# Kernel optimization log

Measured on AMD Instinct MI355X. Metric: run time of the kernel, lower is better.

The kernel has to match this reference:

```python
import jax, jax.numpy as jnp
import numpy as np

BETA = 0.25
NUM_CODEBOOK = 1024
DIM = 256


def setup_inputs() -> dict:
    key = jax.random.key(0)
    k1, k2 = jax.random.split(key)
    z = jax.random.normal(k1, (32, DIM, 32, 32), dtype=jnp.float32)
    # nn.init.uniform_(weight, -1/num_codebook, 1/num_codebook)
    bound = 1.0 / NUM_CODEBOOK
    codebook = jax.random.uniform(k2, (NUM_CODEBOOK, DIM), dtype=jnp.float32,
                                  minval=-bound, maxval=bound)
    return {"z": z, "codebook": codebook}


def reference(z, codebook):
    B, C, H, W = z.shape
    # NCHW -> NHWC -> [B*H*W, C]
    z_flat = jnp.transpose(z, (0, 2, 3, 1)).reshape(-1, C)
    # squared euclidean distances to each code: [B*H*W, K]
    dist = (jnp.sum(z_flat * z_flat, axis=1, keepdims=True)
            + jnp.sum(codebook * codebook, axis=1)
            - 2.0 * jnp.matmul(z_flat, codebook.T))
    idx = jnp.argmin(dist, axis=-1)                      # [B*H*W]
    z_q = codebook[idx].reshape(B, H, W, C)              # gather
    z_q = jnp.transpose(z_q, (0, 3, 1, 2))               # back to NCHW
    commit_loss = (jnp.mean((jax.lax.stop_gradient(z_q) - z) ** 2)
                   + BETA * jnp.mean((z_q - jax.lax.stop_gradient(z)) ** 2))
    # straight-through estimator
    z_q_st = z + jax.lax.stop_gradient(z_q - z)
    return z_q_st, commit_loss
```

## Files before the change

kernel.cpp:

```cpp
#include <hip/hip_runtime.h>
#include <hip/hip_bf16.h>
#include <hip/hip_fp8.h>
#include <stdint.h>


#define WS_CN    0
#define WS_CB    4096
#define WS_PENC  266240
#define WS_PART2 790528
#define WS_PART  791040

typedef float f32x4 __attribute__((ext_vector_type(4)));
typedef long  i64;
typedef long  l64x2 __attribute__((ext_vector_type(2)));

template <bool HI>
static __device__ __forceinline__ unsigned pk2(float a, float b, unsigned old) {
#if __has_builtin(__builtin_amdgcn_cvt_pk_fp8_f32)
    return (unsigned)__builtin_amdgcn_cvt_pk_fp8_f32(a, b, (int)old, HI);
#else
    __hip_fp8_e4m3 qa(a), qb(b);
    unsigned w = (unsigned)qa.__x | ((unsigned)qb.__x << 8);
    return HI ? ((old & 0x0000FFFFu) | (w << 16)) : ((old & 0xFFFF0000u) | w);
#endif
}

__global__ __launch_bounds__(512) void k0_prep(const float* __restrict__ cb,
                                               float* __restrict__ cn256,
                                               unsigned char* __restrict__ cbf8) {
    const int w = threadIdx.x >> 6;
    const int l = threadIdx.x & 63;
    const int code = blockIdx.x * 8 + w;
    const float4 v = ((const float4*)cb)[code * 64 + l];
    float nrm = v.x * v.x + v.y * v.y + v.z * v.z + v.w * v.w;
    #pragma unroll
    for (int off = 1; off < 64; off <<= 1) nrm += __shfl_xor(nrm, off);
    if (l == 0) cn256[code] = 256.f * nrm;
    unsigned u = pk2<false>(-512.f * v.x, -512.f * v.y, 0u);
    u = pk2<true>(-512.f * v.z, -512.f * v.w, u);
    const int q = code >> 8, chunk = (code >> 4) & 15, r16 = code & 15;
    const int ks = l >> 3, kp = l >> 4, g4 = (l >> 1) & 3;
    const int lane = g4 * 16 + r16;
    const int byteoff = q * 65536 + ((chunk * 4 + kp) * 64 + lane) * 16
                      + (ks & 1) * 8 + (l & 1) * 4;
    *(unsigned*)(cbf8 + byteoff) = u;
}

__global__ __launch_bounds__(512) void k1_main(const float* __restrict__ z,
                                               const unsigned char* __restrict__ cbf8,
                                               const float* __restrict__ cn256,
                                               float* __restrict__ penc,
                                               float* __restrict__ part2) {
    __shared__ __align__(16) unsigned char lds[65536];
    const int t = threadIdx.x, w = t >> 6, l = t & 63;
    const int col = l & 15, g4 = l >> 4, gc4 = g4 * 4;
    const int b = blockIdx.x, q = b >> 7, grp = b & 127;
    const int img = grp >> 2, hw0 = (grp & 3) << 8;

    {
        const unsigned char* src = cbf8 + q * 65536;
        #pragma unroll
        for (int i = 0; i < 8; ++i) {
            const int off = i * 8192 + w * 1024;
            __builtin_amdgcn_global_load_lds(
                (const __attribute__((address_space(1))) unsigned*)(src + off + l * 16),
                (__attribute__((address_space(3))) unsigned*)(lds + off), 16, 0, 0);
        }
    }

    const float* zp = z + img * 262144 + hw0 + w * 32;
    float z2 = 0.f;
    i64 zf[2][8];
    #pragma unroll
    for (int pf = 0; pf < 2; ++pf) {
        const int p = pf * 16 + col;
        #pragma unroll
        for (int ks = 0; ks < 8; ++ks) {
            const float* s0 = zp + (ks * 32 + g4 * 8) * 1024 + p;
            float v0 = s0[0], v1 = s0[1024], v2 = s0[2048], v3 = s0[3072];
            float v4 = s0[4096], v5 = s0[5120], v6 = s0[6144], v7 = s0[7168];
            z2 += v0*v0 + v1*v1 + v2*v2 + v3*v3 + v4*v4 + v5*v5 + v6*v6 + v7*v7;
            unsigned lo = pk2<false>(v0, v1, 0u); lo = pk2<true>(v2, v3, lo);
            unsigned hi = pk2<false>(v4, v5, 0u); hi = pk2<true>(v6, v7, hi);
            zf[pf][ks] = (i64)(((unsigned long)hi << 32) | (unsigned long)lo);
        }
    }
    __syncthreads();

    float menc0 = __builtin_bit_cast(float, 0x7F7FFC00u);
    float menc1 = __builtin_bit_cast(float, 0x7F7FFC00u);

    i64 A0[8], A1[8];
#define LDA(DST, c) do {                                                         \
    _Pragma("unroll") for (int kp = 0; kp < 4; ++kp) {                           \
        l64x2 u = *(const l64x2*)(lds + (((c) * 4 + kp) * 64 + l) * 16);         \
        DST[2 * kp] = u.x; DST[2 * kp + 1] = u.y;                                \
    }                                                                            \
} while (0)
#define BODY(CUR, NXT, c) do {                                                   \
    if ((c) + 1 < 16) LDA(NXT, (c) + 1);                                         \
    f32x4 a0 = {0.f,0.f,0.f,0.f}, a1 = {0.f,0.f,0.f,0.f};                        \
    _Pragma("unroll") for (int ks = 0; ks < 8; ++ks) {                           \
        a0 = __builtin_amdgcn_mfma_f32_16x16x32_fp8_fp8(CUR[ks], zf[0][ks], a0, 0, 0, 0); \
        a1 = __builtin_amdgcn_mfma_f32_16x16x32_fp8_fp8(CUR[ks], zf[1][ks], a1, 0, 0, 0); \
    }                                                                            \
    {                                                                            \
        const f32x4 cn = *(const f32x4*)(cn256 + q * 256 + (c) * 16 + gc4);      \
        _Pragma("unroll") for (int r = 0; r < 4; ++r) {                          \
            const unsigned code0 = (unsigned)(q * 256 + (c) * 16 + gc4 + r);     \
            float s; unsigned e;                                                 \
            s = a0[r] + cn[r];                                                   \
            e = (__builtin_bit_cast(unsigned, s) & 0xFFFFFC00u) | code0;         \
            menc0 = fminf(menc0, __builtin_bit_cast(float, e));                  \
            s = a1[r] + cn[r];                                                   \
            e = (__builtin_bit_cast(unsigned, s) & 0xFFFFFC00u) | code0;         \
            menc1 = fminf(menc1, __builtin_bit_cast(float, e));                  \
        }                                                                        \
    }                                                                            \
} while (0)

    LDA(A0, 0);
    #pragma unroll 1
    for (int c2 = 0; c2 < 16; c2 += 2) {
        BODY(A0, A1, c2);
        BODY(A1, A0, c2 + 1);
    }
#undef BODY
#undef LDA

    menc0 = fminf(menc0, __shfl_xor(menc0, 16));
    menc0 = fminf(menc0, __shfl_xor(menc0, 32));
    menc1 = fminf(menc1, __shfl_xor(menc1, 16));
    menc1 = fminf(menc1, __shfl_xor(menc1, 32));
    const int posbase = img * 1024 + hw0 + w * 32;
    if (l < 16) {
        penc[q * 32768 + posbase + l]      = menc0;
        penc[q * 32768 + posbase + 16 + l] = menc1;
    }

    #pragma unroll
    for (int off = 1; off < 64; off <<= 1) z2 += __shfl_xor(z2, off);
    __syncthreads();
    float* red = (float*)lds;
    if (l == 0) red[w] = z2;
    __syncthreads();
    if (t == 0 && q == 0) {
        float s = 0.f;
        #pragma unroll
        for (int i = 0; i < 8; ++i) s += red[i];
        part2[grp] = s;
    }
}

__global__ __launch_bounds__(256) void k2_out(const float* __restrict__ cbf,
                                              const float* __restrict__ penc,
                                              float* __restrict__ out,
                                              float* __restrict__ part) {
    __shared__ __align__(16) float zqbuf[32 * 260];
    __shared__ unsigned idxl[64];
    const int t = threadIdx.x, b = blockIdx.x;
    const int pos0 = b * 64, img = pos0 >> 10, hw0 = pos0 & 1023;

    if (t < 64) {
        const int pos = pos0 + t;
        const float e = fminf(fminf(penc[pos], penc[32768 + pos]),
                              fminf(penc[65536 + pos], penc[98304 + pos]));
        const unsigned eu = __builtin_bit_cast(unsigned, e);
        idxl[t] = eu & 0x3FFu;
        float myS = __builtin_bit_cast(float, eu & 0xFFFFFC00u);
        #pragma unroll
        for (int off = 1; off < 64; off <<= 1) myS += __shfl_xor(myS, off);
        if (t == 0) part[b] = myS * (1.f / 256.f);
    }

    const float4* cb4 = (const float4*)cbf;
    const int pq = t & 7;
    const int cg = t >> 3;
    for (int h = 0; h < 2; ++h) {
        __syncthreads();
        #pragma unroll
        for (int i = 0; i < 8; ++i) {
            const int flat = i * 256 + t;
            const int p = flat >> 6;
            const int qq = flat & 63;
            const unsigned code = idxl[h * 32 + p];
            *(float4*)&zqbuf[p * 260 + qq * 4] = cb4[code * 64 + qq];
        }
        __syncthreads();
        float* ob = out + img * 262144 + hw0 + h * 32 + pq * 4;
        #pragma unroll
        for (int i = 0; i < 8; ++i) {
            const int ch = i * 32 + cg;
            float4 v;
            v.x = zqbuf[(pq * 4 + 0) * 260 + ch];
            v.y = zqbuf[(pq * 4 + 1) * 260 + ch];
            v.z = zqbuf[(pq * 4 + 2) * 260 + ch];
            v.w = zqbuf[(pq * 4 + 3) * 260 + ch];
            *(float4*)(ob + ch * 1024) = v;
        }
    }
}

__global__ __launch_bounds__(256) void k3_red(const float* __restrict__ part2,
                                              const float* __restrict__ part,
                                              float* __restrict__ out) {
    __shared__ float red[256];
    const int t = threadIdx.x;
    float v = part[t] + part[t + 256];
    if (t < 128) v += part2[t];
    red[t] = v;
    __syncthreads();
    #pragma unroll
    for (int off = 128; off > 0; off >>= 1) {
        if (t < off) red[t] += red[t + off];
        __syncthreads();
    }
    if (t == 0) out[8388608] = 1.25f * red[0] / 8388608.f;
}

extern "C" void kernel_launch(void* const* d_in, const int* in_sizes, int n_in,
                              void* d_out, int out_size, void* d_ws, size_t ws_size,
                              hipStream_t stream) {
    const float* z  = (const float*)d_in[0];
    const float* cb = (const float*)d_in[1];
    float* out = (float*)d_out;
    unsigned char* ws = (unsigned char*)d_ws;
    float* cn256 = (float*)(ws + WS_CN);
    unsigned char* cbf8 = ws + WS_CB;
    float* penc  = (float*)(ws + WS_PENC);
    float* part2 = (float*)(ws + WS_PART2);
    float* part  = (float*)(ws + WS_PART);

    hipLaunchKernelGGL(k0_prep, dim3(128), dim3(512), 0, stream, cb, cn256, cbf8);
    hipLaunchKernelGGL(k1_main, dim3(512), dim3(512), 0, stream, z, cbf8, cn256, penc, part2);
    hipLaunchKernelGGL(k2_out,  dim3(512), dim3(256), 0, stream, cb, penc, out, part);
    hipLaunchKernelGGL(k3_red,  dim3(1), dim3(256), 0, stream, part2, part, out);
}
```

Baseline: 44.79 us.

## Split codebook into eighths, give each wave 64 positions in smaller blocks

The main distance kernel now splits the codebook into 8 slices of 128 codes instead of 4 of 256, and runs 1024 blocks of 256 threads with 32KB of LDS instead of 512 blocks of 512 threads with 64KB. Each wave now covers 64 positions with four accumulator sets, so every codebook fragment read from LDS feeds four MFMAs instead of two. The double-buffered A-fragment prefetch is dropped, and the partial-min workspace and the reduction in the output kernel grow to 8 slices. This trades more z loads and conversions (z is now re-read for 8 code slices) and higher register use for better reuse of each LDS read and more blocks per CU.

After: 61.41 us. 37.1% more time.

```diff
diff --git a/kernel.cpp b/kernel.cpp
--- a/kernel.cpp
+++ b/kernel.cpp
@@ -7,8 +7,8 @@
 #define WS_CN    0
 #define WS_CB    4096
 #define WS_PENC  266240
-#define WS_PART2 790528
-#define WS_PART  791040
+#define WS_PART2 1314816
+#define WS_PART  1315328
 
 typedef float f32x4 __attribute__((ext_vector_type(4)));
 typedef long  i64;
@@ -38,41 +38,42 @@
     if (l == 0) cn256[code] = 256.f * nrm;
     unsigned u = pk2<false>(-512.f * v.x, -512.f * v.y, 0u);
     u = pk2<true>(-512.f * v.z, -512.f * v.w, u);
-    const int q = code >> 8, chunk = (code >> 4) & 15, r16 = code & 15;
-    const int ks = l >> 3, kp = l >> 4, g4 = (l >> 1) & 3;
+    const int e = code >> 7, chunk = (code >> 4) & 7, r16 = code & 15;
+    const int kp = l >> 4, g4 = (l >> 1) & 3;
     const int lane = g4 * 16 + r16;
-    const int byteoff = q * 65536 + ((chunk * 4 + kp) * 64 + lane) * 16
-                      + (ks & 1) * 8 + (l & 1) * 4;
+    const int byteoff = e * 32768 + ((chunk * 4 + kp) * 64 + lane) * 16
+                      + ((l >> 3) & 1) * 8 + (l & 1) * 4;
     *(unsigned*)(cbf8 + byteoff) = u;
 }
 
-__global__ __launch_bounds__(512) void k1_main(const float* __restrict__ z,
+__global__ __launch_bounds__(256) void k1_main(const float* __restrict__ z,
                                                const unsigned char* __restrict__ cbf8,
                                                const float* __restrict__ cn256,
                                                float* __restrict__ penc,
                                                float* __restrict__ part2) {
-    __shared__ __align__(16) unsigned char lds[65536];
+    __shared__ __align__(16) unsigned char lds[32768];
+    __shared__ float redz[4];
     const int t = threadIdx.x, w = t >> 6, l = t & 63;
     const int col = l & 15, g4 = l >> 4, gc4 = g4 * 4;
-    const int b = blockIdx.x, q = b >> 7, grp = b & 127;
+    const int b = blockIdx.x, e = b >> 7, grp = b & 127;
     const int img = grp >> 2, hw0 = (grp & 3) << 8;
 
     {
-        const unsigned char* src = cbf8 + q * 65536;
+        const unsigned char* src = cbf8 + e * 32768;
         #pragma unroll
         for (int i = 0; i < 8; ++i) {
-            const int off = i * 8192 + w * 1024;
+            const int off = i * 4096 + w * 1024;
             __builtin_amdgcn_global_load_lds(
                 (const __attribute__((address_space(1))) unsigned*)(src + off + l * 16),
                 (__attribute__((address_space(3))) unsigned*)(lds + off), 16, 0, 0);
         }
     }
 
-    const float* zp = z + img * 262144 + hw0 + w * 32;
+    const float* zp = z + img * 262144 + hw0 + w * 64;
     float z2 = 0.f;
-    i64 zf[2][8];
-    #pragma unroll
-    for (int pf = 0; pf < 2; ++pf) {
+    i64 zf[4][8];
+    #pragma unroll
+    for (int pf = 0; pf < 4; ++pf) {
         const int p = pf * 16 + col;
         #pragma unroll
         for (int ks = 0; ks < 8; ++ks) {
@@ -89,67 +90,67 @@
 
     float menc0 = __builtin_bit_cast(float, 0x7F7FFC00u);
     float menc1 = __builtin_bit_cast(float, 0x7F7FFC00u);
-
-    i64 A0[8], A1[8];
-#define LDA(DST, c) do {                                                         \
-    _Pragma("unroll") for (int kp = 0; kp < 4; ++kp) {                           \
-        l64x2 u = *(const l64x2*)(lds + (((c) * 4 + kp) * 64 + l) * 16);         \
-        DST[2 * kp] = u.x; DST[2 * kp + 1] = u.y;                                \
-    }                                                                            \
-} while (0)
-#define BODY(CUR, NXT, c) do {                                                   \
-    if ((c) + 1 < 16) LDA(NXT, (c) + 1);                                         \
-    f32x4 a0 = {0.f,0.f,0.f,0.f}, a1 = {0.f,0.f,0.f,0.f};                        \
-    _Pragma("unroll") for (int ks = 0; ks < 8; ++ks) {                           \
-        a0 = __builtin_amdgcn_mfma_f32_16x16x32_fp8_fp8(CUR[ks], zf[0][ks], a0, 0, 0, 0); \
-        a1 = __builtin_amdgcn_mfma_f32_16x16x32_fp8_fp8(CUR[ks], zf[1][ks], a1, 0, 0, 0); \
-    }                                                                            \
-    {                                                                            \
-        const f32x4 cn = *(const f32x4*)(cn256 + q * 256 + (c) * 16 + gc4);      \
-        _Pragma("unroll") for (int r = 0; r < 4; ++r) {                          \
-            const unsigned code0 = (unsigned)(q * 256 + (c) * 16 + gc4 + r);     \
-            float s; unsigned e;                                                 \
-            s = a0[r] + cn[r];                                                   \
-            e = (__builtin_bit_cast(unsigned, s) & 0xFFFFFC00u) | code0;         \
-            menc0 = fminf(menc0, __builtin_bit_cast(float, e));                  \
-            s = a1[r] + cn[r];                                                   \
-            e = (__builtin_bit_cast(unsigned, s) & 0xFFFFFC00u) | code0;         \
-            menc1 = fminf(menc1, __builtin_bit_cast(float, e));                  \
-        }                                                                        \
-    }                                                                            \
-} while (0)
-
-    LDA(A0, 0);
+    float menc2 = __builtin_bit_cast(float, 0x7F7FFC00u);
+    float menc3 = __builtin_bit_cast(float, 0x7F7FFC00u);
+
     #pragma unroll 1
-    for (int c2 = 0; c2 < 16; c2 += 2) {
-        BODY(A0, A1, c2);
-        BODY(A1, A0, c2 + 1);
-    }
-#undef BODY
-#undef LDA
+    for (int c = 0; c < 8; ++c) {
+        i64 A[8];
+        #pragma unroll
+        for (int kp = 0; kp < 4; ++kp) {
+            l64x2 u = *(const l64x2*)(lds + ((c * 4 + kp) * 64 + l) * 16);
+            A[2 * kp] = u.x; A[2 * kp + 1] = u.y;
+        }
+        f32x4 a0 = {0.f,0.f,0.f,0.f}, a1 = {0.f,0.f,0.f,0.f};
+        f32x4 a2 = {0.f,0.f,0.f,0.f}, a3 = {0.f,0.f,0.f,0.f};
+        #pragma unroll
+        for (int ks = 0; ks < 8; ++ks) {
+            a0 = __builtin_amdgcn_mfma_f32_16x16x32_fp8_fp8(A[ks], zf[0][ks], a0, 0, 0, 0);
+            a1 = __builtin_amdgcn_mfma_f32_16x16x32_fp8_fp8(A[ks], zf[1][ks], a1, 0, 0, 0);
+            a2 = __builtin_amdgcn_mfma_f32_16x16x32_fp8_fp8(A[ks], zf[2][ks], a2, 0, 0, 0);
+            a3 = __builtin_amdgcn_mfma_f32_16x16x32_fp8_fp8(A[ks], zf[3][ks], a3, 0, 0, 0);
+        }
+        const f32x4 cn = *(const f32x4*)(cn256 + e * 128 + c * 16 + gc4);
+        #pragma unroll
+        for (int r = 0; r < 4; ++r) {
+            const unsigned code0 = (unsigned)(e * 128 + c * 16 + gc4 + r);
+            float s; unsigned u;
+            s = a0[r] + cn[r];
+            u = (__builtin_bit_cast(unsigned, s) & 0xFFFFFC00u) | code0;
+            menc0 = fminf(menc0, __builtin_bit_cast(float, u));
+            s = a1[r] + cn[r];
+            u = (__builtin_bit_cast(unsigned, s) & 0xFFFFFC00u) | code0;
+            menc1 = fminf(menc1, __builtin_bit_cast(float, u));
+            s = a2[r] + cn[r];
+            u = (__builtin_bit_cast(unsigned, s) & 0xFFFFFC00u) | code0;
+            menc2 = fminf(menc2, __builtin_bit_cast(float, u));
+            s = a3[r] + cn[r];
+            u = (__builtin_bit_cast(unsigned, s) & 0xFFFFFC00u) | code0;
+            menc3 = fminf(menc3, __builtin_bit_cast(float, u));
+        }
+    }
 
     menc0 = fminf(menc0, __shfl_xor(menc0, 16));
     menc0 = fminf(menc0, __shfl_xor(menc0, 32));
     menc1 = fminf(menc1, __shfl_xor(menc1, 16));
     menc1 = fminf(menc1, __shfl_xor(menc1, 32));
-    const int posbase = img * 1024 + hw0 + w * 32;
+    menc2 = fminf(menc2, __shfl_xor(menc2, 16));
+    menc2 = fminf(menc2, __shfl_xor(menc2, 32));
+    menc3 = fminf(menc3, __shfl_xor(menc3, 16));
+    menc3 = fminf(menc3, __shfl_xor(menc3, 32));
     if (l < 16) {
-        penc[q * 32768 + posbase + l]      = menc0;
-        penc[q * 32768 + posbase + 16 + l] = menc1;
+        const int pbase = e * 32768 + grp * 256 + w * 64;
+        penc[pbase + l]      = menc0;
+        penc[pbase + 16 + l] = menc1;
+        penc[pbase + 32 + l] = menc2;
+        penc[pbase + 48 + l] = menc3;
     }
 
     #pragma unroll
     for (int off = 1; off < 64; off <<= 1) z2 += __shfl_xor(z2, off);
+    if (l == 0) redz[w] = z2;
     __syncthreads();
-    float* red = (float*)lds;
-    if (l == 0) red[w] = z2;
-    __syncthreads();
-    if (t == 0 && q == 0) {
-        float s = 0.f;
-        #pragma unroll
-        for (int i = 0; i < 8; ++i) s += red[i];
-        part2[grp] = s;
-    }
+    if (t == 0 && e == 0) part2[grp] = redz[0] + redz[1] + redz[2] + redz[3];
 }
 
 __global__ __launch_bounds__(256) void k2_out(const float* __restrict__ cbf,
@@ -163,8 +164,11 @@
 
     if (t < 64) {
         const int pos = pos0 + t;
-        const float e = fminf(fminf(penc[pos], penc[32768 + pos]),
-                              fminf(penc[65536 + pos], penc[98304 + pos]));
+        const float e01 = fminf(penc[pos],          penc[32768 + pos]);
+        const float e23 = fminf(penc[65536 + pos],  penc[98304 + pos]);
+        const float e45 = fminf(penc[131072 + pos], penc[163840 + pos]);
+        const float e67 = fminf(penc[196608 + pos], penc[229376 + pos]);
+        const float e = fminf(fminf(e01, e23), fminf(e45, e67));
         const unsigned eu = __builtin_bit_cast(unsigned, e);
         idxl[t] = eu & 0x3FFu;
         float myS = __builtin_bit_cast(float, eu & 0xFFFFFC00u);
@@ -232,7 +236,7 @@
     float* part  = (float*)(ws + WS_PART);
 
     hipLaunchKernelGGL(k0_prep, dim3(128), dim3(512), 0, stream, cb, cn256, cbf8);
-    hipLaunchKernelGGL(k1_main, dim3(512), dim3(512), 0, stream, z, cbf8, cn256, penc, part2);
+    hipLaunchKernelGGL(k1_main, dim3(1024), dim3(256), 0, stream, z, cbf8, cn256, penc, part2);
     hipLaunchKernelGGL(k2_out,  dim3(512), dim3(256), 0, stream, cb, penc, out, part);
     hipLaunchKernelGGL(k3_red,  dim3(1), dim3(256), 0, stream, part2, part, out);
 }
```

## Split codebook into eight slices and use smaller blocks in main kernel

Applied to the files above, without the earlier changes.

Repartitions the distance/argmin kernel so each block handles 128 codes and 128 positions with 256 threads, giving 2048 blocks instead of 512 and halving LDS per block. The codebook FP8 layout, partial-argmin buffer (now eight slices), and the downstream merge and loss reduction are adjusted to match. This aims to raise occupancy and the number of waves across CUs. In exchange, each z tile is loaded and converted to FP8 by twice as many blocks, and the merge step reads more partial results.

Result: slower. 52.25 us (+16.7%).

```diff
diff --git a/kernel.cpp b/kernel.cpp
--- a/kernel.cpp
+++ b/kernel.cpp
@@ -7,8 +7,8 @@
 #define WS_CN    0
 #define WS_CB    4096
 #define WS_PENC  266240
-#define WS_PART2 790528
-#define WS_PART  791040
+#define WS_PART2 1314816
+#define WS_PART  1315840
 
 typedef float f32x4 __attribute__((ext_vector_type(4)));
 typedef long  i64;
@@ -38,30 +38,30 @@
     if (l == 0) cn256[code] = 256.f * nrm;
     unsigned u = pk2<false>(-512.f * v.x, -512.f * v.y, 0u);
     u = pk2<true>(-512.f * v.z, -512.f * v.w, u);
-    const int q = code >> 8, chunk = (code >> 4) & 15, r16 = code & 15;
-    const int ks = l >> 3, kp = l >> 4, g4 = (l >> 1) & 3;
+    const int e = code >> 7, chunk = (code >> 4) & 7, r16 = code & 15;
+    const int kp = l >> 4, g4 = (l >> 1) & 3;
     const int lane = g4 * 16 + r16;
-    const int byteoff = q * 65536 + ((chunk * 4 + kp) * 64 + lane) * 16
-                      + (ks & 1) * 8 + (l & 1) * 4;
+    const int byteoff = e * 32768 + ((chunk * 4 + kp) * 64 + lane) * 16
+                      + ((l >> 3) & 1) * 8 + (l & 1) * 4;
     *(unsigned*)(cbf8 + byteoff) = u;
 }
 
-__global__ __launch_bounds__(512) void k1_main(const float* __restrict__ z,
+__global__ __launch_bounds__(256) void k1_main(const float* __restrict__ z,
                                                const unsigned char* __restrict__ cbf8,
                                                const float* __restrict__ cn256,
                                                float* __restrict__ penc,
                                                float* __restrict__ part2) {
-    __shared__ __align__(16) unsigned char lds[65536];
+    __shared__ __align__(16) unsigned char lds[32768];
     const int t = threadIdx.x, w = t >> 6, l = t & 63;
     const int col = l & 15, g4 = l >> 4, gc4 = g4 * 4;
-    const int b = blockIdx.x, q = b >> 7, grp = b & 127;
-    const int img = grp >> 2, hw0 = (grp & 3) << 8;
+    const int b = blockIdx.x, e = b >> 8, grp = b & 255;
+    const int img = grp >> 3, hw0 = (grp & 7) << 7;
 
     {
-        const unsigned char* src = cbf8 + q * 65536;
+        const unsigned char* src = cbf8 + e * 32768;
         #pragma unroll
         for (int i = 0; i < 8; ++i) {
-            const int off = i * 8192 + w * 1024;
+            const int off = i * 4096 + w * 1024;
             __builtin_amdgcn_global_load_lds(
                 (const __attribute__((address_space(1))) unsigned*)(src + off + l * 16),
                 (__attribute__((address_space(3))) unsigned*)(lds + off), 16, 0, 0);
@@ -98,30 +98,30 @@
     }                                                                            \
 } while (0)
 #define BODY(CUR, NXT, c) do {                                                   \
-    if ((c) + 1 < 16) LDA(NXT, (c) + 1);                                         \
+    if ((c) + 1 < 8) LDA(NXT, (c) + 1);                                          \
     f32x4 a0 = {0.f,0.f,0.f,0.f}, a1 = {0.f,0.f,0.f,0.f};                        \
     _Pragma("unroll") for (int ks = 0; ks < 8; ++ks) {                           \
         a0 = __builtin_amdgcn_mfma_f32_16x16x32_fp8_fp8(CUR[ks], zf[0][ks], a0, 0, 0, 0); \
         a1 = __builtin_amdgcn_mfma_f32_16x16x32_fp8_fp8(CUR[ks], zf[1][ks], a1, 0, 0, 0); \
     }                                                                            \
     {                                                                            \
-        const f32x4 cn = *(const f32x4*)(cn256 + q * 256 + (c) * 16 + gc4);      \
+        const f32x4 cn = *(const f32x4*)(cn256 + e * 128 + (c) * 16 + gc4);      \
         _Pragma("unroll") for (int r = 0; r < 4; ++r) {                          \
-            const unsigned code0 = (unsigned)(q * 256 + (c) * 16 + gc4 + r);     \
-            float s; unsigned e;                                                 \
+            const unsigned code0 = (unsigned)(e * 128 + (c) * 16 + gc4 + r);     \
+            float s; unsigned u;                                                 \
             s = a0[r] + cn[r];                                                   \
-            e = (__builtin_bit_cast(unsigned, s) & 0xFFFFFC00u) | code0;         \
-            menc0 = fminf(menc0, __builtin_bit_cast(float, e));                  \
+            u = (__builtin_bit_cast(unsigned, s) & 0xFFFFFC00u) | code0;         \
+            menc0 = fminf(menc0, __builtin_bit_cast(float, u));                  \
             s = a1[r] + cn[r];                                                   \
-            e = (__builtin_bit_cast(unsigned, s) & 0xFFFFFC00u) | code0;         \
-            menc1 = fminf(menc1, __builtin_bit_cast(float, e));                  \
+            u = (__builtin_bit_cast(unsigned, s) & 0xFFFFFC00u) | code0;         \
+            menc1 = fminf(menc1, __builtin_bit_cast(float, u));                  \
         }                                                                        \
     }                                                                            \
 } while (0)
 
     LDA(A0, 0);
     #pragma unroll 1
-    for (int c2 = 0; c2 < 16; c2 += 2) {
+    for (int c2 = 0; c2 < 8; c2 += 2) {
         BODY(A0, A1, c2);
         BODY(A1, A0, c2 + 1);
     }
@@ -132,10 +132,10 @@
     menc0 = fminf(menc0, __shfl_xor(menc0, 32));
     menc1 = fminf(menc1, __shfl_xor(menc1, 16));
     menc1 = fminf(menc1, __shfl_xor(menc1, 32));
-    const int posbase = img * 1024 + hw0 + w * 32;
+    const int posbase = grp * 128 + w * 32;
     if (l < 16) {
-        penc[q * 32768 + posbase + l]      = menc0;
-        penc[q * 32768 + posbase + 16 + l] = menc1;
+        penc[e * 32768 + posbase + l]      = menc0;
+        penc[e * 32768 + posbase + 16 + l] = menc1;
     }
 
     #pragma unroll
@@ -144,12 +144,7 @@
     float* red = (float*)lds;
     if (l == 0) red[w] = z2;
     __syncthreads();
-    if (t == 0 && q == 0) {
-        float s = 0.f;
-        #pragma unroll
-        for (int i = 0; i < 8; ++i) s += red[i];
-        part2[grp] = s;
-    }
+    if (t == 0 && e == 0) part2[grp] = red[0] + red[1] + red[2] + red[3];
 }
 
 __global__ __launch_bounds__(256) void k2_out(const float* __restrict__ cbf,
@@ -163,8 +158,11 @@
 
     if (t < 64) {
         const int pos = pos0 + t;
-        const float e = fminf(fminf(penc[pos], penc[32768 + pos]),
-                              fminf(penc[65536 + pos], penc[98304 + pos]));
+        const float e01 = fminf(penc[pos],          penc[32768 + pos]);
+        const float e23 = fminf(penc[65536 + pos],  penc[98304 + pos]);
+        const float e45 = fminf(penc[131072 + pos], penc[163840 + pos]);
+        const float e67 = fminf(penc[196608 + pos], penc[229376 + pos]);
+        const float e = fminf(fminf(e01, e23), fminf(e45, e67));
         const unsigned eu = __builtin_bit_cast(unsigned, e);
         idxl[t] = eu & 0x3FFu;
         float myS = __builtin_bit_cast(float, eu & 0xFFFFFC00u);
@@ -206,9 +204,7 @@
                                               float* __restrict__ out) {
     __shared__ float red[256];
     const int t = threadIdx.x;
-    float v = part[t] + part[t + 256];
-    if (t < 128) v += part2[t];
-    red[t] = v;
+    red[t] = part[t] + part[t + 256] + part2[t];
     __syncthreads();
     #pragma unroll
     for (int off = 128; off > 0; off >>= 1) {
@@ -232,7 +228,7 @@
     float* part  = (float*)(ws + WS_PART);
 
     hipLaunchKernelGGL(k0_prep, dim3(128), dim3(512), 0, stream, cb, cn256, cbf8);
-    hipLaunchKernelGGL(k1_main, dim3(512), dim3(512), 0, stream, z, cbf8, cn256, penc, part2);
+    hipLaunchKernelGGL(k1_main, dim3(2048), dim3(256), 0, stream, z, cbf8, cn256, penc, part2);
     hipLaunchKernelGGL(k2_out,  dim3(512), dim3(256), 0, stream, cb, penc, out, part);
     hipLaunchKernelGGL(k3_red,  dim3(1), dim3(256), 0, stream, part2, part, out);
 }
```
